# Performance work log

Measured on AMD Instinct MI355X. Metric: run time of the kernel, lower is better.

## Reference

```python
import math
import jax, jax.numpy as jnp
import numpy as np
from jax import lax

EPS = 1e-5


def setup_inputs() -> dict:
    key = jax.random.key(0)
    ks = jax.random.split(key, 12)
    B, L, C = 4, 4096, 512
    d_inner, d_state, d_conv = 2 * C, 4, 4
    dt_rank = math.ceil(C / 16)  # 32
    s = 0.02
    A = jnp.tile(jnp.arange(1, d_state + 1, dtype=jnp.float32), (d_inner, 1))
    return {
        "hidden_states": jax.random.normal(ks[0], (B, L, C), jnp.float32),
        "mask": jnp.zeros((B, L), jnp.int32),
        "residual": jax.random.normal(ks[1], (B, L, C), jnp.float32),
        "norm_weight": jnp.ones((C,), jnp.float32),
        "conv_w": jax.random.normal(ks[2], (C, C, 3, 3), jnp.float32) * s,
        "conv_b": jnp.zeros((C,), jnp.float32),
        "in_proj_w": jax.random.normal(ks[3], (2 * d_inner, C), jnp.float32) * s,
        "conv1d_w": jax.random.normal(ks[4], (d_inner, 1, d_conv), jnp.float32) * s,
        "conv1d_b": jnp.zeros((d_inner,), jnp.float32),
        "x_proj_w": jax.random.normal(ks[5], (dt_rank + 2 * d_state, d_inner), jnp.float32) * s,
        "dt_proj_w": jax.random.normal(ks[6], (d_inner, dt_rank), jnp.float32) * s,
        "dt_proj_b": jnp.full((d_inner,), -4.6, jnp.float32),  # softplus ~ 0.01
        "A_log": jnp.log(A),
        "D": jnp.ones((d_inner,), jnp.float32),
        "out_proj_w": jax.random.normal(ks[7], (C, 2 * C), jnp.float32) * s,
    }


def _mamba(u, in_proj_w, conv1d_w, conv1d_b, x_proj_w, dt_proj_w, dt_proj_b, A_log, D, out_proj_w):
    # u: [B, L, C]
    Bn, Ln, _ = u.shape
    d_inner = conv1d_w.shape[0]
    d_state = A_log.shape[1]
    dt_rank = dt_proj_w.shape[1]
    d_conv = conv1d_w.shape[-1]
    xz = jnp.einsum("blc,ec->ble", u, in_proj_w)  # [B,L,2*d_inner]
    x, z = jnp.split(xz, 2, axis=-1)
    # causal depthwise conv1d (left pad d_conv-1)
    xc = lax.conv_general_dilated(
        x.transpose(0, 2, 1), conv1d_w, (1,), ((d_conv - 1, 0),),
        feature_group_count=d_inner, dimension_numbers=("NCH", "OIH", "NCH"))
    x = jax.nn.silu((xc + conv1d_b[None, :, None]).transpose(0, 2, 1))  # [B,L,D]
    x_dbl = jnp.einsum("bld,ed->ble", x, x_proj_w)
    dtr, Bm, Cm = jnp.split(x_dbl, [dt_rank, dt_rank + d_state], axis=-1)
    dt = jax.nn.softplus(jnp.einsum("blr,dr->bld", dtr, dt_proj_w) + dt_proj_b)
    A = -jnp.exp(A_log)  # [D,N]
    dA = jnp.exp(dt[..., None] * A)                              # [B,L,D,N]
    dBx = dt[..., None] * Bm[:, :, None, :] * x[..., None]       # [B,L,D,N]

    def step(h, t):
        dA_t, dBx_t, C_t = t
        h = dA_t * h + dBx_t
        return h, jnp.einsum("bdn,bn->bd", h, C_t)

    h0 = jnp.zeros((Bn, d_inner, d_state), dt.dtype)
    _, ys = lax.scan(step, h0, (dA.transpose(1, 0, 2, 3), dBx.transpose(1, 0, 2, 3), Cm.transpose(1, 0, 2)))
    y = ys.transpose(1, 0, 2) + x * D
    y = y * jax.nn.silu(z)
    return jnp.einsum("bld,cd->blc", y, out_proj_w)


def reference(hidden_states, mask, residual, norm_weight, conv_w, conv_b,
              in_proj_w, conv1d_w, conv1d_b, x_proj_w, dt_proj_w, dt_proj_b,
              A_log, D, out_proj_w):
    # fused add + RMSNorm, prenorm, residual in fp32
    res = (hidden_states + residual).astype(jnp.float32)
    var = jnp.mean(res * res, axis=-1, keepdims=True)
    hs = res * lax.rsqrt(var + EPS) * norm_weight
    Bn, Ln, Cn = hs.shape
    Ls = int(round(math.sqrt(Ln)))
    img = hs.transpose(0, 2, 1).reshape(Bn, Cn, Ls, Ls)
    img = lax.conv_general_dilated(img, conv_w, (1, 1), ((1, 1), (1, 1)),
                                   dimension_numbers=("NCHW", "OIHW", "NCHW"))
    img = img + conv_b[None, :, None, None]
    hs = img.reshape(Bn, Cn, Ln).transpose(0, 2, 1)  # [B,L,C]
    # gather tokens where mask==0 (equal count per row; here n_easy = L)
    n_easy = Ln
    order = jnp.argsort(mask, axis=1, stable=True)
    easy_idx = order[:, :n_easy]  # [B, n_easy]
    easy = jnp.take_along_axis(hs, easy_idx[:, :, None], axis=1)
    mixed = _mamba(easy, in_proj_w, conv1d_w, conv1d_b, x_proj_w,
                   dt_proj_w, dt_proj_b, A_log, D, out_proj_w)
    # scatter mixer output back into the full sequence
    x = hs.at[jnp.arange(Bn)[:, None], easy_idx].set(mixed)
    return x, res
```

## Files before the change

kernel.cpp:

```cpp
#include <hip/hip_runtime.h>
#include <hip/hip_bf16.h>

#define BB 4
#define LL 4096
#define CC 512
#define DI 1024
#define DS 4
#define DR 32
#define LS 64
#define CHUNK 64
#define NCH 64
#define PW 66

typedef unsigned short ushortT;
typedef __attribute__((ext_vector_type(8))) short bf16x8;
typedef __attribute__((ext_vector_type(4))) float f32x4;

static __device__ __forceinline__ float b2f(ushortT u) {
    union { unsigned int i; float f; } v; v.i = ((unsigned int)u) << 16; return v.f;
}
static __device__ __forceinline__ ushortT f2b(float f) {
    unsigned int x = __float_as_uint(f);
    unsigned int lsb = (x >> 16) & 1u;
    x += 0x7fffu + lsb;
    return (ushortT)(x >> 16);
}

static __device__ __forceinline__ void gl16(const ushortT* g, ushortT* l) {
    typedef const __attribute__((address_space(1))) unsigned int GU;
    typedef __attribute__((address_space(3))) unsigned int LU;
    __builtin_amdgcn_global_load_lds((GU*)(unsigned long long)(const void*)g,
                                     (LU*)(unsigned int)(unsigned long long)(void*)l,
                                     16, 0, 0);
}

__global__ __launch_bounds__(512) void k_norm(const float* __restrict__ hid,
                                              const float* __restrict__ resi,
                                              const float* __restrict__ nw,
                                              float* __restrict__ out_res,
                                              ushortT* __restrict__ himg) {
    int bl = blockIdx.x;
    int c  = threadIdx.x;
    size_t base = (size_t)bl * CC;
    float h = hid[base + c] + resi[base + c];
    out_res[base + c] = h;

    float s = h * h;
    #pragma unroll
    for (int o = 32; o > 0; o >>= 1) s += __shfl_xor(s, o);
    __shared__ float ws[8];
    int w = c >> 6;
    if ((c & 63) == 0) ws[w] = s;
    __syncthreads();
    float tot = 0.f;
    #pragma unroll
    for (int i = 0; i < 8; i++) tot += ws[i];
    float scale = rsqrtf(tot / (float)CC + 1e-5f);

    int b = bl >> 12, l = bl & 4095;
    int iy = (l >> 6) + 1, ix = (l & 63) + 1;
    himg[(((size_t)b * PW + iy) * PW + ix) * CC + c] = f2b(h * scale * nw[c]);
}

__global__ __launch_bounds__(256) void k_prep1(const float* __restrict__ convw,
                                               const float* __restrict__ inw,
                                               ushortT* __restrict__ wb3,
                                               ushortT* __restrict__ wbi) {
    int blk = blockIdx.x, tid = threadIdx.x;
    if (blk < 1024) {
        int g = blk * 256 + tid;
        int ic = g & 511, oc = g >> 9;
        const float* src = convw + ((size_t)(oc * CC + ic)) * 9;
        #pragma unroll
        for (int tap = 0; tap < 9; tap++)
            wb3[((size_t)oc * 9 + tap) * 512 + ic] = f2b(src[tap]);
    } else {
        int i = (blk - 1024) * 256 + tid;
        float4 v = ((const float4*)inw)[i];
        ushort4 o = { f2b(v.x), f2b(v.y), f2b(v.z), f2b(v.w) };
        ((ushort4*)wbi)[i] = o;
    }
}

__global__ __launch_bounds__(256) void k_prep2(const float* __restrict__ outw,
                                               const float* __restrict__ xpw,
                                               const float* __restrict__ dtw,
                                               ushortT* __restrict__ wbo,
                                               ushortT* __restrict__ wbx,
                                               ushortT* __restrict__ dtwb) {
    int blk = blockIdx.x, tid = threadIdx.x;
    if (blk < 512) {
        int i = blk * 256 + tid;
        float4 v = ((const float4*)outw)[i];
        ushort4 o = { f2b(v.x), f2b(v.y), f2b(v.z), f2b(v.w) };
        ((ushort4*)wbo)[i] = o;
    } else if (blk < 768) {
        int g = (blk - 512) * 256 + tid;
        int k = g & 1023, e = g >> 10;
        wbx[g] = (e < 40) ? f2b(xpw[(size_t)e * DI + k]) : (ushortT)0;
    } else {
        int i = (blk - 768) * 256 + tid;
        float4 v = ((const float4*)dtw)[i];
        ushort4 o = { f2b(v.x), f2b(v.y), f2b(v.z), f2b(v.w) };
        ((ushort4*)dtwb)[i] = o;
    }
}

__global__ __launch_bounds__(256) void k_conv2d_mfma(const ushortT* __restrict__ himg,
                                                     const ushortT* __restrict__ wb3,
                                                     const float* __restrict__ convb,
                                                     ushortT* __restrict__ u) {
    const int b = blockIdx.z;
    const int ytile = blockIdx.x;
    const int n0 = blockIdx.y * 128;
    const int tid = threadIdx.x;
    const int lane = tid & 63, w = tid >> 6;
    const int wr = w >> 1, wc = w & 1;
    const int fm = lane & 15, kg = lane >> 4;

    __shared__ __align__(16) ushortT As[128][32];
    __shared__ __align__(16) ushortT Bs[128][32];

    f32x4 acc[4][4];
    #pragma unroll
    for (int i = 0; i < 4; i++)
        #pragma unroll
        for (int j = 0; j < 4; j++) acc[i][j] = (f32x4){0.f, 0.f, 0.f, 0.f};

    const int sp  = (lane >> 2);
    const int sch = (((lane & 3) ^ ((sp >> 1) & 3))) * 8;
    const int rc  = (kg ^ ((fm >> 1) & 3)) * 8;

    for (int tap = 0; tap < 9; tap++) {
        const int dy = tap / 3 - 1, dx = tap % 3 - 1;
        size_t ag[2], bg[2];
        #pragma unroll
        for (int q = 0; q < 2; q++) {
            int p  = w * 32 + q * 16 + sp;
            int iy = ytile * 2 + (p >> 6) + dy + 1;
            int ix = (p & 63) + dx + 1;
            ag[q] = (((size_t)b * PW + iy) * PW + ix) * CC + sch;
            bg[q] = ((size_t)(n0 + p) * 9 + tap) * 512 + sch;
        }
        for (int ics = 0; ics < 16; ics++) {
            const int ko = ics * 32;
            #pragma unroll
            for (int q = 0; q < 2; q++) {
                gl16(himg + ag[q] + ko, &As[w * 32 + q * 16][0]);
                gl16(wb3  + bg[q] + ko, &Bs[w * 32 + q * 16][0]);
            }
            __syncthreads();
            bf16x8 afr[4], bfr[4];
            #pragma unroll
            for (int ms = 0; ms < 4; ms++)
                afr[ms] = *(const bf16x8*)(&As[wr * 64 + ms * 16 + fm][rc]);
            #pragma unroll
            for (int ns = 0; ns < 4; ns++)
                bfr[ns] = *(const bf16x8*)(&Bs[wc * 64 + ns * 16 + fm][rc]);
            #pragma unroll
            for (int ms = 0; ms < 4; ms++)
                #pragma unroll
                for (int ns = 0; ns < 4; ns++)
                    acc[ms][ns] = __builtin_amdgcn_mfma_f32_16x16x32_bf16(afr[ms], bfr[ns], acc[ms][ns], 0, 0, 0);
            __syncthreads();
        }
    }

    const int rowb = ytile * 128 + wr * 64;
    const int colb = n0 + wc * 64;
    #pragma unroll
    for (int ms = 0; ms < 4; ms++) {
        #pragma unroll
        for (int ns = 0; ns < 4; ns++) {
            int col = colb + ns * 16 + fm;
            float bias = convb[col];
            f32x4 v = acc[ms][ns];
            #pragma unroll
            for (int r = 0; r < 4; r++) {
                int row = rowb + ms * 16 + kg * 4 + r;
                u[((size_t)(b * LL + row)) * CC + col] = f2b(v[r] + bias);
            }
        }
    }
}

__global__ __launch_bounds__(256) void k_inproj_mfma(const ushortT* __restrict__ A,
                                                     const ushortT* __restrict__ Wb,
                                                     ushortT* __restrict__ xout,
                                                     ushortT* __restrict__ zout) {
    const int m0 = blockIdx.x * 128, n0 = blockIdx.y * 128;
    const int tid = threadIdx.x;
    const int lane = tid & 63, w = tid >> 6;
    const int wr = w >> 1, wc = w & 1;
    const int fm = lane & 15, kg = lane >> 4;

    __shared__ __align__(16) ushortT As[128][32];
    __shared__ __align__(16) ushortT Bs[128][32];

    f32x4 acc[4][4];
    #pragma unroll
    for (int i = 0; i < 4; i++)
        #pragma unroll
        for (int j = 0; j < 4; j++) acc[i][j] = (f32x4){0.f, 0.f, 0.f, 0.f};

    const int sp  = (lane >> 2);
    const int sch = (((lane & 3) ^ ((sp >> 1) & 3))) * 8;
    const int rc  = (kg ^ ((fm >> 1) & 3)) * 8;

    for (int k0 = 0; k0 < CC; k0 += 32) {
        #pragma unroll
        for (int q = 0; q < 2; q++) {
            int p = w * 32 + q * 16 + sp;
            gl16(A  + (size_t)(m0 + p) * CC + k0 + sch, &As[w * 32 + q * 16][0]);
            gl16(Wb + (size_t)(n0 + p) * CC + k0 + sch, &Bs[w * 32 + q * 16][0]);
        }
        __syncthreads();
        bf16x8 afr[4], bfr[4];
        #pragma unroll
        for (int ms = 0; ms < 4; ms++)
            afr[ms] = *(const bf16x8*)(&As[wr * 64 + ms * 16 + fm][rc]);
        #pragma unroll
        for (int ns = 0; ns < 4; ns++)
            bfr[ns] = *(const bf16x8*)(&Bs[wc * 64 + ns * 16 + fm][rc]);
        #pragma unroll
        for (int ms = 0; ms < 4; ms++)
            #pragma unroll
            for (int ns = 0; ns < 4; ns++)
                acc[ms][ns] = __builtin_amdgcn_mfma_f32_16x16x32_bf16(afr[ms], bfr[ns], acc[ms][ns], 0, 0, 0);
        __syncthreads();
    }

    const int rowb = m0 + wr * 64;
    const int colb = n0 + wc * 64;
    #pragma unroll
    for (int ms = 0; ms < 4; ms++) {
        #pragma unroll
        for (int ns = 0; ns < 4; ns++) {
            int col = colb + ns * 16 + fm;
            f32x4 v = acc[ms][ns];
            #pragma unroll
            for (int r = 0; r < 4; r++) {
                int row = rowb + ms * 16 + kg * 4 + r;
                float val = v[r];
                if (col < DI) {
                    xout[(size_t)row * DI + col] = f2b(val);
                } else {
                    float s = val / (1.f + __expf(-val));
                    zout[(size_t)row * DI + (col - DI)] = f2b(s);
                }
            }
        }
    }
}

__global__ __launch_bounds__(256) void k_outproj_mfma(const ushortT* __restrict__ A,
                                                      const ushortT* __restrict__ Wb,
                                                      float* __restrict__ out) {
    const int m0 = blockIdx.x * 128, n0 = blockIdx.y * 128;
    const int tid = threadIdx.x;
    const int lane = tid & 63, w = tid >> 6;
    const int wr = w >> 1, wc = w & 1;
    const int fm = lane & 15, kg = lane >> 4;

    __shared__ __align__(16) ushortT As[128][32];
    __shared__ __align__(16) ushortT Bs[128][32];

    f32x4 acc[4][4];
    #pragma unroll
    for (int i = 0; i < 4; i++)
        #pragma unroll
        for (int j = 0; j < 4; j++) acc[i][j] = (f32x4){0.f, 0.f, 0.f, 0.f};

    const int sp  = (lane >> 2);
    const int sch = (((lane & 3) ^ ((sp >> 1) & 3))) * 8;
    const int rc  = (kg ^ ((fm >> 1) & 3)) * 8;

    for (int k0 = 0; k0 < DI; k0 += 32) {
        #pragma unroll
        for (int q = 0; q < 2; q++) {
            int p = w * 32 + q * 16 + sp;
            gl16(A  + (size_t)(m0 + p) * DI + k0 + sch, &As[w * 32 + q * 16][0]);
            gl16(Wb + (size_t)(n0 + p) * DI + k0 + sch, &Bs[w * 32 + q * 16][0]);
        }
        __syncthreads();
        bf16x8 afr[4], bfr[4];
        #pragma unroll
        for (int ms = 0; ms < 4; ms++)
            afr[ms] = *(const bf16x8*)(&As[wr * 64 + ms * 16 + fm][rc]);
        #pragma unroll
        for (int ns = 0; ns < 4; ns++)
            bfr[ns] = *(const bf16x8*)(&Bs[wc * 64 + ns * 16 + fm][rc]);
        #pragma unroll
        for (int ms = 0; ms < 4; ms++)
            #pragma unroll
            for (int ns = 0; ns < 4; ns++)
                acc[ms][ns] = __builtin_amdgcn_mfma_f32_16x16x32_bf16(afr[ms], bfr[ns], acc[ms][ns], 0, 0, 0);
        __syncthreads();
    }

    const int rowb = m0 + wr * 64;
    const int colb = n0 + wc * 64;
    #pragma unroll
    for (int ms = 0; ms < 4; ms++) {
        #pragma unroll
        for (int ns = 0; ns < 4; ns++) {
            int col = colb + ns * 16 + fm;
            f32x4 v = acc[ms][ns];
            #pragma unroll
            for (int r = 0; r < 4; r++) {
                int row = rowb + ms * 16 + kg * 4 + r;
                out[(size_t)row * CC + col] = v[r];
            }
        }
    }
}

__global__ __launch_bounds__(256) void k_xproj_mfma(const ushortT* __restrict__ A,
                                                    const ushortT* __restrict__ Wb,
                                                    float* __restrict__ xdbl,
                                                    ushortT* __restrict__ dtr_b) {
    const int m0 = blockIdx.x * 128;
    const int tid = threadIdx.x;
    const int lane = tid & 63, w = tid >> 6;
    const int wr = w >> 1, wc = w & 1;
    const int fm = lane & 15, kg = lane >> 4;

    __shared__ ushortT As[128][40];
    __shared__ ushortT Bs[64][40];

    f32x4 acc[4][2];
    #pragma unroll
    for (int i = 0; i < 4; i++)
        #pragma unroll
        for (int j = 0; j < 2; j++) acc[i][j] = (f32x4){0.f, 0.f, 0.f, 0.f};

    const int ar = tid >> 2;
    const int lcol = (tid & 3) * 8;

    for (int k0 = 0; k0 < DI; k0 += 32) {
        #pragma unroll
        for (int q = 0; q < 2; q++) {
            int r = ar + q * 64;
            bf16x8 av = *(const bf16x8*)(A + (size_t)(m0 + r) * DI + k0 + lcol);
            *(bf16x8*)(&As[r][lcol]) = av;
        }
        {
            bf16x8 bv = *(const bf16x8*)(Wb + (size_t)ar * DI + k0 + lcol);
            *(bf16x8*)(&Bs[ar][lcol]) = bv;
        }
        __syncthreads();
        bf16x8 afr[4], bfr[2];
        #pragma unroll
        for (int ms = 0; ms < 4; ms++)
            afr[ms] = *(const bf16x8*)(&As[wr * 64 + ms * 16 + fm][kg * 8]);
        #pragma unroll
        for (int ns = 0; ns < 2; ns++)
            bfr[ns] = *(const bf16x8*)(&Bs[wc * 32 + ns * 16 + fm][kg * 8]);
        #pragma unroll
        for (int ms = 0; ms < 4; ms++)
            #pragma unroll
            for (int ns = 0; ns < 2; ns++)
                acc[ms][ns] = __builtin_amdgcn_mfma_f32_16x16x32_bf16(afr[ms], bfr[ns], acc[ms][ns], 0, 0, 0);
        __syncthreads();
    }

    const int rowb = m0 + wr * 64;
    #pragma unroll
    for (int ms = 0; ms < 4; ms++) {
        #pragma unroll
        for (int ns = 0; ns < 2; ns++) {
            int col = wc * 32 + ns * 16 + fm;
            f32x4 v = acc[ms][ns];
            #pragma unroll
            for (int r = 0; r < 4; r++) {
                int row = rowb + ms * 16 + kg * 4 + r;
                float val = v[r];
                if (col < 40) xdbl[(size_t)row * 40 + col] = val;
                if (col < 32) dtr_b[(size_t)row * 32 + col] = f2b(val);
            }
        }
    }
}

__global__ __launch_bounds__(256) void k_dt_mfma(const ushortT* __restrict__ Ab,
                                                 const ushortT* __restrict__ Wb,
                                                 const float* __restrict__ dtb,
                                                 ushortT* __restrict__ dty) {
    const int m0 = blockIdx.x * 128, n0 = blockIdx.y * 128;
    const int tid = threadIdx.x;
    const int lane = tid & 63, w = tid >> 6;
    const int wr = w >> 1, wc = w & 1;
    const int fm = lane & 15, kg = lane >> 4;

    __shared__ ushortT As[128][40];
    __shared__ ushortT Bs[128][40];

    f32x4 acc[4][4];
    #pragma unroll
    for (int i = 0; i < 4; i++)
        #pragma unroll
        for (int j = 0; j < 4; j++) acc[i][j] = (f32x4){0.f, 0.f, 0.f, 0.f};

    const int ar = tid >> 2;
    const int lcol = (tid & 3) * 8;
    #pragma unroll
    for (int q = 0; q < 2; q++) {
        int r = ar + q * 64;
        bf16x8 av = *(const bf16x8*)(Ab + (size_t)(m0 + r) * 32 + lcol);
        bf16x8 bv = *(const bf16x8*)(Wb + (size_t)(n0 + r) * 32 + lcol);
        *(bf16x8*)(&As[r][lcol]) = av;
        *(bf16x8*)(&Bs[r][lcol]) = bv;
    }
    __syncthreads();
    bf16x8 afr[4], bfr[4];
    #pragma unroll
    for (int ms = 0; ms < 4; ms++)
        afr[ms] = *(const bf16x8*)(&As[wr * 64 + ms * 16 + fm][kg * 8]);
    #pragma unroll
    for (int ns = 0; ns < 4; ns++)
        bfr[ns] = *(const bf16x8*)(&Bs[wc * 64 + ns * 16 + fm][kg * 8]);
    #pragma unroll
    for (int ms = 0; ms < 4; ms++)
        #pragma unroll
        for (int ns = 0; ns < 4; ns++)
            acc[ms][ns] = __builtin_amdgcn_mfma_f32_16x16x32_bf16(afr[ms], bfr[ns], acc[ms][ns], 0, 0, 0);

    const int rowb = m0 + wr * 64;
    const int colb = n0 + wc * 64;
    #pragma unroll
    for (int ms = 0; ms < 4; ms++) {
        #pragma unroll
        for (int ns = 0; ns < 4; ns++) {
            int col = colb + ns * 16 + fm;
            float bias = dtb[col];
            f32x4 v = acc[ms][ns];
            #pragma unroll
            for (int r = 0; r < 4; r++) {
                int row = rowb + ms * 16 + kg * 4 + r;
                float a = v[r] + bias;
                float sp = (a > 20.f) ? a : log1pf(__expf(a));
                dty[(size_t)row * DI + col] = f2b(sp);
            }
        }
    }
}

__global__ __launch_bounds__(256) void k_conv1d(const ushortT* __restrict__ xbuf,
                                                const float* __restrict__ w,
                                                const float* __restrict__ bias,
                                                ushortT* __restrict__ xs) {
    int idx = blockIdx.x * 256 + threadIdx.x;
    int d = idx & (DI - 1);
    int l = (idx >> 10) & (LL - 1);
    int b = idx >> 22;
    float acc = bias[d];
    #pragma unroll
    for (int k = 0; k < 4; k++) {
        int ll = l + k - 3;
        if (ll >= 0)
            acc += b2f(xbuf[(((size_t)(b << 12) + ll) << 10) + d]) * w[d * 4 + k];
    }
    float s = acc / (1.f + __expf(-acc));
    xs[idx] = f2b(s);
}

__global__ __launch_bounds__(256) void k_scan_p1(const ushortT* __restrict__ dt,
                                                 const ushortT* __restrict__ xs,
                                                 const float* __restrict__ xdbl,
                                                 const float* __restrict__ alog,
                                                 float* __restrict__ P,
                                                 float* __restrict__ S) {
    int d  = blockIdx.x * 256 + threadIdx.x;
    int ch = blockIdx.y;
    int b  = blockIdx.z;
    int t  = threadIdx.x;

    __shared__ float sB[CHUNK][4];
    if (t < CHUNK) {
        const float* xr = xdbl + ((size_t)(b * LL + ch * CHUNK + t)) * 40;
        float4 v = *(const float4*)(xr + 32);
        sB[t][0] = v.x; sB[t][1] = v.y; sB[t][2] = v.z; sB[t][3] = v.w;
    }
    __syncthreads();

    float An[4], h[4] = {0.f, 0.f, 0.f, 0.f}, Pp[4] = {1.f, 1.f, 1.f, 1.f};
    #pragma unroll
    for (int n = 0; n < 4; n++) An[n] = -__expf(alog[d * 4 + n]);

    size_t row0 = (size_t)b * LL + ch * CHUNK;
    for (int i = 0; i < CHUNK; i++) {
        size_t row = row0 + i;
        float dtv = b2f(dt[row * DI + d]);
        float xv  = b2f(xs[row * DI + d]);
        float dbx = dtv * xv;
        #pragma unroll
        for (int n = 0; n < 4; n++) {
            float dA = __expf(dtv * An[n]);
            h[n]  = dA * h[n] + dbx * sB[i][n];
            Pp[n] *= dA;
        }
    }
    size_t o = (((size_t)b * NCH + ch) * DI + d) * 4;
    *(float4*)(P + o) = make_float4(Pp[0], Pp[1], Pp[2], Pp[3]);
    *(float4*)(S + o) = make_float4(h[0], h[1], h[2], h[3]);
}

__global__ __launch_bounds__(256) void k_scan_cmb(const float* __restrict__ P,
                                                  const float* __restrict__ S,
                                                  float* __restrict__ Hin) {
    int td = blockIdx.x * 256 + threadIdx.x;
    int b = td >> 10, d = td & (DI - 1);
    float h[4] = {0.f, 0.f, 0.f, 0.f};
    for (int ch = 0; ch < NCH; ch++) {
        size_t o = (((size_t)b * NCH + ch) * DI + d) * 4;
        *(float4*)(Hin + o) = make_float4(h[0], h[1], h[2], h[3]);
        float4 p = *(const float4*)(P + o);
        float4 s = *(const float4*)(S + o);
        h[0] = p.x * h[0] + s.x;
        h[1] = p.y * h[1] + s.y;
        h[2] = p.z * h[2] + s.z;
        h[3] = p.w * h[3] + s.w;
    }
}

__global__ __launch_bounds__(256) void k_scan_p2(ushortT* dty,
                                                 const ushortT* __restrict__ xs,
                                                 const float* __restrict__ xdbl,
                                                 const ushortT* __restrict__ zs,
                                                 const float* __restrict__ alog,
                                                 const float* __restrict__ Dv,
                                                 const float* __restrict__ Hin) {
    int d  = blockIdx.x * 256 + threadIdx.x;
    int ch = blockIdx.y;
    int b  = blockIdx.z;
    int t  = threadIdx.x;

    __shared__ float sBC[CHUNK][8];
    if (t < CHUNK) {
        const float* xr = xdbl + ((size_t)(b * LL + ch * CHUNK + t)) * 40;
        float4 v1 = *(const float4*)(xr + 32);
        float4 v2 = *(const float4*)(xr + 36);
        sBC[t][0] = v1.x; sBC[t][1] = v1.y; sBC[t][2] = v1.z; sBC[t][3] = v1.w;
        sBC[t][4] = v2.x; sBC[t][5] = v2.y; sBC[t][6] = v2.z; sBC[t][7] = v2.w;
    }
    __syncthreads();

    float An[4];
    #pragma unroll
    for (int n = 0; n < 4; n++) An[n] = -__expf(alog[d * 4 + n]);
    float Dd = Dv[d];

    size_t o = (((size_t)b * NCH + ch) * DI + d) * 4;
    float4 h0 = *(const float4*)(Hin + o);
    float h[4] = {h0.x, h0.y, h0.z, h0.w};

    size_t row0 = (size_t)b * LL + ch * CHUNK;
    for (int i = 0; i < CHUNK; i++) {
        size_t row = row0 + i;
        float dtv = b2f(dty[row * DI + d]);
        float xv  = b2f(xs[row * DI + d]);
        float dbx = dtv * xv;
        float y = 0.f;
        #pragma unroll
        for (int n = 0; n < 4; n++) {
            float dA = __expf(dtv * An[n]);
            h[n] = dA * h[n] + dbx * sBC[i][n];
            y += h[n] * sBC[i][4 + n];
        }
        float sz = b2f(zs[row * DI + d]);
        dty[row * DI + d] = f2b((y + xv * Dd) * sz);
    }
}

__global__ __launch_bounds__(256) void k_sentinel(float* __restrict__ out0) {
    int i = blockIdx.x * 256 + threadIdx.x;
    out0[i] = 1.0f;
}

extern "C" void kernel_launch(void* const* d_in, const int* in_sizes, int n_in,
                              void* d_out, int out_size, void* d_ws, size_t ws_size,
                              hipStream_t stream) {
    const float* hid   = (const float*)d_in[0];
    const float* resi  = (const float*)d_in[2];
    const float* nw    = (const float*)d_in[3];
    const float* convw = (const float*)d_in[4];
    const float* convb = (const float*)d_in[5];
    const float* inw   = (const float*)d_in[6];
    const float* c1w   = (const float*)d_in[7];
    const float* c1b   = (const float*)d_in[8];
    const float* xpw   = (const float*)d_in[9];
    const float* dtw   = (const float*)d_in[10];
    const float* dtb   = (const float*)d_in[11];
    const float* alog  = (const float*)d_in[12];
    const float* Dv    = (const float*)d_in[13];
    const float* outw  = (const float*)d_in[14];

    float* out0 = (float*)d_out;
    float* out1 = out0 + (size_t)BB * LL * CC;

    const size_t RA = (size_t)BB * LL * CC * 2;
    const size_t RB = (size_t)BB * LL * DI * 2;
    const size_t NEED = RA + 2 * RB;
    const size_t HIMG_BYTES = (size_t)BB * PW * PW * CC * 2;

    ushortT* himg  = (ushortT*)d_out;
    ushortT* wbi   = (ushortT*)((char*)d_out + (18u << 20));
    ushortT* xs    = (ushortT*)d_out;
    char* base = (char*)d_ws;
    ushortT* u     = (ushortT*)base;
    float*   xdbl  = (float*)base;
    ushortT* wbx   = (ushortT*)(base + 2621440);
    ushortT* dtwb  = (ushortT*)(base + 2752512);
    ushortT* wbo   = (ushortT*)(base + (3u << 20));
    float*   Pbuf  = (float*)(base + (4u << 20));
    ushortT* dtr_b = (ushortT*)(base + (4u << 20));
    float*   Sbuf  = (float*)(base + (8u << 20));
    float*   Hin   = (float*)(base + (12u << 20));
    ushortT* wb3   = (ushortT*)(base + RA);
    ushortT* xb    = (ushortT*)(base + RA);
    ushortT* dty   = (ushortT*)(base + RA);
    ushortT* zsilu = (ushortT*)(base + RA + RB);

    if (ws_size < NEED) {
        k_sentinel<<<(BB * LL * CC) / 256, 256, 0, stream>>>(out0);
        return;
    }

    hipMemsetAsync(himg, 0, HIMG_BYTES, stream);
    k_norm<<<BB * LL, 512, 0, stream>>>(hid, resi, nw, out1, himg);
    k_prep1<<<2048, 256, 0, stream>>>(convw, inw, wb3, wbi);
    k_conv2d_mfma<<<dim3(32, 4, BB), 256, 0, stream>>>(himg, wb3, convb, u);
    k_inproj_mfma<<<dim3(128, 16), 256, 0, stream>>>(u, wbi, xb, zsilu);
    k_prep2<<<800, 256, 0, stream>>>(outw, xpw, dtw, wbo, wbx, dtwb);
    k_conv1d<<<65536, 256, 0, stream>>>(xb, c1w, c1b, xs);
    k_xproj_mfma<<<128, 256, 0, stream>>>(xs, wbx, xdbl, dtr_b);
    k_dt_mfma<<<dim3(128, 8), 256, 0, stream>>>(dtr_b, dtwb, dtb, dty);
    k_scan_p1<<<dim3(DI / 256, NCH, BB), 256, 0, stream>>>(dty, xs, xdbl, alog, Pbuf, Sbuf);
    k_scan_cmb<<<(BB * DI) / 256, 256, 0, stream>>>(Pbuf, Sbuf, Hin);
    k_scan_p2<<<dim3(DI / 256, NCH, BB), 256, 0, stream>>>(dty, xs, xdbl, zsilu, alog, Dv, Hin);
    k_outproj_mfma<<<dim3(128, 4), 256, 0, stream>>>(dty, wbo, out0);
}
```

Before: 429.0 us.

## Widen GEMM K-tile to 64 and retile x_proj for more blocks

The conv2d, in_proj and out_proj MFMA GEMMs now stage 64-wide K slices in LDS instead of 32, using a new 8-way XOR swizzle. Each barrier pair therefore covers two MFMA K-steps, which halves the number of syncs and load rounds. The x_proj GEMM is retiled to 64-row blocks with one warp per 16 rows, using async global-to-LDS loads and twice as many blocks, to improve parallelism. LDS use per block doubles for the large GEMMs, which may reduce occupancy.

```diff
diff --git a/kernel.cpp b/kernel.cpp
--- a/kernel.cpp
+++ b/kernel.cpp
@@ -118,8 +118,8 @@
     const int wr = w >> 1, wc = w & 1;
     const int fm = lane & 15, kg = lane >> 4;
 
-    __shared__ __align__(16) ushortT As[128][32];
-    __shared__ __align__(16) ushortT Bs[128][32];
+    __shared__ __align__(16) ushortT As[128][64];
+    __shared__ __align__(16) ushortT Bs[128][64];
 
     f32x4 acc[4][4];
     #pragma unroll
@@ -127,41 +127,44 @@
         #pragma unroll
         for (int j = 0; j < 4; j++) acc[i][j] = (f32x4){0.f, 0.f, 0.f, 0.f};
 
-    const int sp  = (lane >> 2);
-    const int sch = (((lane & 3) ^ ((sp >> 1) & 3))) * 8;
-    const int rc  = (kg ^ ((fm >> 1) & 3)) * 8;
+    const int sp8 = lane >> 3;
+    const int sch = ((lane & 7) ^ sp8) * 8;
 
     for (int tap = 0; tap < 9; tap++) {
         const int dy = tap / 3 - 1, dx = tap % 3 - 1;
-        size_t ag[2], bg[2];
-        #pragma unroll
-        for (int q = 0; q < 2; q++) {
-            int p  = w * 32 + q * 16 + sp;
+        size_t ag[4], bg[4];
+        #pragma unroll
+        for (int j = 0; j < 4; j++) {
+            int p  = w * 32 + j * 8 + sp8;
             int iy = ytile * 2 + (p >> 6) + dy + 1;
             int ix = (p & 63) + dx + 1;
-            ag[q] = (((size_t)b * PW + iy) * PW + ix) * CC + sch;
-            bg[q] = ((size_t)(n0 + p) * 9 + tap) * 512 + sch;
-        }
-        for (int ics = 0; ics < 16; ics++) {
-            const int ko = ics * 32;
-            #pragma unroll
-            for (int q = 0; q < 2; q++) {
-                gl16(himg + ag[q] + ko, &As[w * 32 + q * 16][0]);
-                gl16(wb3  + bg[q] + ko, &Bs[w * 32 + q * 16][0]);
+            ag[j] = (((size_t)b * PW + iy) * PW + ix) * CC + sch;
+            bg[j] = ((size_t)(n0 + p) * 9 + tap) * 512 + sch;
+        }
+        for (int ics = 0; ics < 8; ics++) {
+            const int ko = ics * 64;
+            #pragma unroll
+            for (int j = 0; j < 4; j++) {
+                gl16(himg + ag[j] + ko, &As[w * 32 + j * 8][0]);
+                gl16(wb3  + bg[j] + ko, &Bs[w * 32 + j * 8][0]);
             }
             __syncthreads();
-            bf16x8 afr[4], bfr[4];
-            #pragma unroll
-            for (int ms = 0; ms < 4; ms++)
-                afr[ms] = *(const bf16x8*)(&As[wr * 64 + ms * 16 + fm][rc]);
-            #pragma unroll
-            for (int ns = 0; ns < 4; ns++)
-                bfr[ns] = *(const bf16x8*)(&Bs[wc * 64 + ns * 16 + fm][rc]);
-            #pragma unroll
-            for (int ms = 0; ms < 4; ms++)
+            #pragma unroll
+            for (int ks = 0; ks < 2; ks++) {
+                const int rc = ((ks * 4 + kg) ^ (fm & 7)) * 8;
+                bf16x8 afr[4], bfr[4];
+                #pragma unroll
+                for (int ms = 0; ms < 4; ms++)
+                    afr[ms] = *(const bf16x8*)(&As[wr * 64 + ms * 16 + fm][rc]);
                 #pragma unroll
                 for (int ns = 0; ns < 4; ns++)
-                    acc[ms][ns] = __builtin_amdgcn_mfma_f32_16x16x32_bf16(afr[ms], bfr[ns], acc[ms][ns], 0, 0, 0);
+                    bfr[ns] = *(const bf16x8*)(&Bs[wc * 64 + ns * 16 + fm][rc]);
+                #pragma unroll
+                for (int ms = 0; ms < 4; ms++)
+                    #pragma unroll
+                    for (int ns = 0; ns < 4; ns++)
+                        acc[ms][ns] = __builtin_amdgcn_mfma_f32_16x16x32_bf16(afr[ms], bfr[ns], acc[ms][ns], 0, 0, 0);
+            }
             __syncthreads();
         }
     }
@@ -194,8 +197,8 @@
     const int wr = w >> 1, wc = w & 1;
     const int fm = lane & 15, kg = lane >> 4;
 
-    __shared__ __align__(16) ushortT As[128][32];
-    __shared__ __align__(16) ushortT Bs[128][32];
+    __shared__ __align__(16) ushortT As[128][64];
+    __shared__ __align__(16) ushortT Bs[128][64];
 
     f32x4 acc[4][4];
     #pragma unroll
@@ -203,30 +206,33 @@
         #pragma unroll
         for (int j = 0; j < 4; j++) acc[i][j] = (f32x4){0.f, 0.f, 0.f, 0.f};
 
-    const int sp  = (lane >> 2);
-    const int sch = (((lane & 3) ^ ((sp >> 1) & 3))) * 8;
-    const int rc  = (kg ^ ((fm >> 1) & 3)) * 8;
-
-    for (int k0 = 0; k0 < CC; k0 += 32) {
-        #pragma unroll
-        for (int q = 0; q < 2; q++) {
-            int p = w * 32 + q * 16 + sp;
-            gl16(A  + (size_t)(m0 + p) * CC + k0 + sch, &As[w * 32 + q * 16][0]);
-            gl16(Wb + (size_t)(n0 + p) * CC + k0 + sch, &Bs[w * 32 + q * 16][0]);
+    const int sp8 = lane >> 3;
+    const int sch = ((lane & 7) ^ sp8) * 8;
+
+    for (int k0 = 0; k0 < CC; k0 += 64) {
+        #pragma unroll
+        for (int j = 0; j < 4; j++) {
+            int p = w * 32 + j * 8 + sp8;
+            gl16(A  + (size_t)(m0 + p) * CC + k0 + sch, &As[w * 32 + j * 8][0]);
+            gl16(Wb + (size_t)(n0 + p) * CC + k0 + sch, &Bs[w * 32 + j * 8][0]);
         }
         __syncthreads();
-        bf16x8 afr[4], bfr[4];
-        #pragma unroll
-        for (int ms = 0; ms < 4; ms++)
-            afr[ms] = *(const bf16x8*)(&As[wr * 64 + ms * 16 + fm][rc]);
-        #pragma unroll
-        for (int ns = 0; ns < 4; ns++)
-            bfr[ns] = *(const bf16x8*)(&Bs[wc * 64 + ns * 16 + fm][rc]);
-        #pragma unroll
-        for (int ms = 0; ms < 4; ms++)
+        #pragma unroll
+        for (int ks = 0; ks < 2; ks++) {
+            const int rc = ((ks * 4 + kg) ^ (fm & 7)) * 8;
+            bf16x8 afr[4], bfr[4];
+            #pragma unroll
+            for (int ms = 0; ms < 4; ms++)
+                afr[ms] = *(const bf16x8*)(&As[wr * 64 + ms * 16 + fm][rc]);
             #pragma unroll
             for (int ns = 0; ns < 4; ns++)
-                acc[ms][ns] = __builtin_amdgcn_mfma_f32_16x16x32_bf16(afr[ms], bfr[ns], acc[ms][ns], 0, 0, 0);
+                bfr[ns] = *(const bf16x8*)(&Bs[wc * 64 + ns * 16 + fm][rc]);
+            #pragma unroll
+            for (int ms = 0; ms < 4; ms++)
+                #pragma unroll
+                for (int ns = 0; ns < 4; ns++)
+                    acc[ms][ns] = __builtin_amdgcn_mfma_f32_16x16x32_bf16(afr[ms], bfr[ns], acc[ms][ns], 0, 0, 0);
+        }
         __syncthreads();
     }
 
@@ -262,8 +268,8 @@
     const int wr = w >> 1, wc = w & 1;
     const int fm = lane & 15, kg = lane >> 4;
 
-    __shared__ __align__(16) ushortT As[128][32];
-    __shared__ __align__(16) ushortT Bs[128][32];
+    __shared__ __align__(16) ushortT As[128][64];
+    __shared__ __align__(16) ushortT Bs[128][64];
 
     f32x4 acc[4][4];
     #pragma unroll
@@ -271,30 +277,33 @@
         #pragma unroll
         for (int j = 0; j < 4; j++) acc[i][j] = (f32x4){0.f, 0.f, 0.f, 0.f};
 
-    const int sp  = (lane >> 2);
-    const int sch = (((lane & 3) ^ ((sp >> 1) & 3))) * 8;
-    const int rc  = (kg ^ ((fm >> 1) & 3)) * 8;
-
-    for (int k0 = 0; k0 < DI; k0 += 32) {
-        #pragma unroll
-        for (int q = 0; q < 2; q++) {
-            int p = w * 32 + q * 16 + sp;
-            gl16(A  + (size_t)(m0 + p) * DI + k0 + sch, &As[w * 32 + q * 16][0]);
-            gl16(Wb + (size_t)(n0 + p) * DI + k0 + sch, &Bs[w * 32 + q * 16][0]);
+    const int sp8 = lane >> 3;
+    const int sch = ((lane & 7) ^ sp8) * 8;
+
+    for (int k0 = 0; k0 < DI; k0 += 64) {
+        #pragma unroll
+        for (int j = 0; j < 4; j++) {
+            int p = w * 32 + j * 8 + sp8;
+            gl16(A  + (size_t)(m0 + p) * DI + k0 + sch, &As[w * 32 + j * 8][0]);
+            gl16(Wb + (size_t)(n0 + p) * DI + k0 + sch, &Bs[w * 32 + j * 8][0]);
         }
         __syncthreads();
-        bf16x8 afr[4], bfr[4];
-        #pragma unroll
-        for (int ms = 0; ms < 4; ms++)
-            afr[ms] = *(const bf16x8*)(&As[wr * 64 + ms * 16 + fm][rc]);
-        #pragma unroll
-        for (int ns = 0; ns < 4; ns++)
-            bfr[ns] = *(const bf16x8*)(&Bs[wc * 64 + ns * 16 + fm][rc]);
-        #pragma unroll
-        for (int ms = 0; ms < 4; ms++)
+        #pragma unroll
+        for (int ks = 0; ks < 2; ks++) {
+            const int rc = ((ks * 4 + kg) ^ (fm & 7)) * 8;
+            bf16x8 afr[4], bfr[4];
+            #pragma unroll
+            for (int ms = 0; ms < 4; ms++)
+                afr[ms] = *(const bf16x8*)(&As[wr * 64 + ms * 16 + fm][rc]);
             #pragma unroll
             for (int ns = 0; ns < 4; ns++)
-                acc[ms][ns] = __builtin_amdgcn_mfma_f32_16x16x32_bf16(afr[ms], bfr[ns], acc[ms][ns], 0, 0, 0);
+                bfr[ns] = *(const bf16x8*)(&Bs[wc * 64 + ns * 16 + fm][rc]);
+            #pragma unroll
+            for (int ms = 0; ms < 4; ms++)
+                #pragma unroll
+                for (int ns = 0; ns < 4; ns++)
+                    acc[ms][ns] = __builtin_amdgcn_mfma_f32_16x16x32_bf16(afr[ms], bfr[ns], acc[ms][ns], 0, 0, 0);
+        }
         __syncthreads();
     }
 
@@ -319,65 +328,47 @@
                                                     const ushortT* __restrict__ Wb,
                                                     float* __restrict__ xdbl,
                                                     ushortT* __restrict__ dtr_b) {
-    const int m0 = blockIdx.x * 128;
+    const int m0 = blockIdx.x * 64;
     const int tid = threadIdx.x;
     const int lane = tid & 63, w = tid >> 6;
-    const int wr = w >> 1, wc = w & 1;
     const int fm = lane & 15, kg = lane >> 4;
 
-    __shared__ ushortT As[128][40];
-    __shared__ ushortT Bs[64][40];
-
-    f32x4 acc[4][2];
-    #pragma unroll
-    for (int i = 0; i < 4; i++)
-        #pragma unroll
-        for (int j = 0; j < 2; j++) acc[i][j] = (f32x4){0.f, 0.f, 0.f, 0.f};
-
-    const int ar = tid >> 2;
-    const int lcol = (tid & 3) * 8;
+    __shared__ __align__(16) ushortT As[64][32];
+    __shared__ __align__(16) ushortT Bs[64][32];
+
+    f32x4 acc[4];
+    #pragma unroll
+    for (int j = 0; j < 4; j++) acc[j] = (f32x4){0.f, 0.f, 0.f, 0.f};
+
+    const int sp  = lane >> 2;
+    const int sch = (((lane & 3) ^ ((sp >> 1) & 3))) * 8;
+    const int rc  = (kg ^ ((fm >> 1) & 3)) * 8;
 
     for (int k0 = 0; k0 < DI; k0 += 32) {
-        #pragma unroll
-        for (int q = 0; q < 2; q++) {
-            int r = ar + q * 64;
-            bf16x8 av = *(const bf16x8*)(A + (size_t)(m0 + r) * DI + k0 + lcol);
-            *(bf16x8*)(&As[r][lcol]) = av;
-        }
-        {
-            bf16x8 bv = *(const bf16x8*)(Wb + (size_t)ar * DI + k0 + lcol);
-            *(bf16x8*)(&Bs[ar][lcol]) = bv;
-        }
+        gl16(A  + (size_t)(m0 + w * 16 + sp) * DI + k0 + sch, &As[w * 16][0]);
+        gl16(Wb + (size_t)(w * 16 + sp) * DI + k0 + sch, &Bs[w * 16][0]);
         __syncthreads();
-        bf16x8 afr[4], bfr[2];
-        #pragma unroll
-        for (int ms = 0; ms < 4; ms++)
-            afr[ms] = *(const bf16x8*)(&As[wr * 64 + ms * 16 + fm][kg * 8]);
-        #pragma unroll
-        for (int ns = 0; ns < 2; ns++)
-            bfr[ns] = *(const bf16x8*)(&Bs[wc * 32 + ns * 16 + fm][kg * 8]);
-        #pragma unroll
-        for (int ms = 0; ms < 4; ms++)
-            #pragma unroll
-            for (int ns = 0; ns < 2; ns++)
-                acc[ms][ns] = __builtin_amdgcn_mfma_f32_16x16x32_bf16(afr[ms], bfr[ns], acc[ms][ns], 0, 0, 0);
+        bf16x8 afr = *(const bf16x8*)(&As[w * 16 + fm][rc]);
+        bf16x8 bfr[4];
+        #pragma unroll
+        for (int ns = 0; ns < 4; ns++)
+            bfr[ns] = *(const bf16x8*)(&Bs[ns * 16 + fm][rc]);
+        #pragma unroll
+        for (int ns = 0; ns < 4; ns++)
+            acc[ns] = __builtin_amdgcn_mfma_f32_16x16x32_bf16(afr, bfr[ns], acc[ns], 0, 0, 0);
         __syncthreads();
     }
 
-    const int rowb = m0 + wr * 64;
-    #pragma unroll
-    for (int ms = 0; ms < 4; ms++) {
-        #pragma unroll
-        for (int ns = 0; ns < 2; ns++) {
-            int col = wc * 32 + ns * 16 + fm;
-            f32x4 v = acc[ms][ns];
-            #pragma unroll
-            for (int r = 0; r < 4; r++) {
-                int row = rowb + ms * 16 + kg * 4 + r;
-                float val = v[r];
-                if (col < 40) xdbl[(size_t)row * 40 + col] = val;
-                if (col < 32) dtr_b[(size_t)row * 32 + col] = f2b(val);
-            }
+    #pragma unroll
+    for (int ns = 0; ns < 4; ns++) {
+        int col = ns * 16 + fm;
+        f32x4 v = acc[ns];
+        #pragma unroll
+        for (int r = 0; r < 4; r++) {
+            int row = m0 + w * 16 + kg * 4 + r;
+            float val = v[r];
+            if (col < 40) xdbl[(size_t)row * 40 + col] = val;
+            if (col < 32) dtr_b[(size_t)row * 32 + col] = f2b(val);
         }
     }
 }
@@ -633,7 +624,7 @@
     k_inproj_mfma<<<dim3(128, 16), 256, 0, stream>>>(u, wbi, xb, zsilu);
     k_prep2<<<800, 256, 0, stream>>>(outw, xpw, dtw, wbo, wbx, dtwb);
     k_conv1d<<<65536, 256, 0, stream>>>(xb, c1w, c1b, xs);
-    k_xproj_mfma<<<128, 256, 0, stream>>>(xs, wbx, xdbl, dtr_b);
+    k_xproj_mfma<<<256, 256, 0, stream>>>(xs, wbx, xdbl, dtr_b);
     k_dt_mfma<<<dim3(128, 8), 256, 0, stream>>>(dtr_b, dtwb, dtb, dty);
     k_scan_p1<<<dim3(DI / 256, NCH, BB), 256, 0, stream>>>(dty, xs, xdbl, alog, Pbuf, Sbuf);
     k_scan_cmb<<<(BB * DI) / 256, 256, 0, stream>>>(Pbuf, Sbuf, Hin);
```

Result: faster. 405.1 us (-5.6%).
